# Optimization experiments

Measured on AMD Instinct MI355X. Metric: run time of the kernel, lower is better.

## Reference

```python
import jax, jax.numpy as jnp
import numpy as np

B, S, D, H = 8, 1024, 768, 12
DH = D // H  # 64
PATCHES = S  # module's `patches` arg; rows >= patches//2 are zeroed pre-softmax


def setup_inputs() -> dict:
    key = jax.random.key(0)
    ks = jax.random.split(key, 5)
    sc = 1.0 / np.sqrt(D)
    return {
        "hidden_states": jax.random.normal(ks[0], (B, S, D), dtype=jnp.float32),
        "Wq": jax.random.normal(ks[1], (D, D), dtype=jnp.float32) * sc,
        "bq": jnp.zeros((D,), dtype=jnp.float32),
        "Wk": jax.random.normal(ks[2], (D, D), dtype=jnp.float32) * sc,
        "bk": jnp.zeros((D,), dtype=jnp.float32),
        "Wv": jax.random.normal(ks[3], (D, D), dtype=jnp.float32) * sc,
        "bv": jnp.zeros((D,), dtype=jnp.float32),
        "Wo": jax.random.normal(ks[4], (D, D), dtype=jnp.float32) * sc,
        "bo": jnp.zeros((D,), dtype=jnp.float32),
    }


def _split_heads(x):
    # [B,S,D] -> [B,H,S,DH]
    b, s, _ = x.shape
    return x.reshape(b, s, H, DH).transpose(0, 2, 1, 3)


def reference(hidden_states, Wq, bq, Wk, bk, Wv, bv, Wo, bo):
    # self-attention path (kv=None), mask=None path, eval-mode dropout (identity)
    q = _split_heads(hidden_states @ Wq + bq)
    k = _split_heads(hidden_states @ Wk + bk)
    v = _split_heads(hidden_states @ Wv + bv)
    scores = jnp.einsum("bhqd,bhkd->bhqk", q, k) / np.sqrt(DH)
    # custom masking: zero out all score rows for query positions >= patches//2
    scores = scores.at[:, :, PATCHES // 2 :, :].set(0.0)
    probs = jax.nn.softmax(scores, axis=-1)
    ctx = jnp.einsum("bhqk,bhkd->bhqd", probs, v)
    ctx = ctx.transpose(0, 2, 1, 3).reshape(hidden_states.shape[0], -1, D)
    return ctx @ Wo + bo  # vis=False -> weights not returned
```

## Files before the change

### kernel.cpp

```cpp
#include <hip/hip_runtime.h>
#include <hip/hip_bf16.h>
#include <cstdint>


typedef __bf16 bf16_t;
typedef bf16_t bf16x8 __attribute__((ext_vector_type(8)));
typedef float f32x4 __attribute__((ext_vector_type(4)));

#define QSCALE 0.18033688011112042f

__device__ __forceinline__ f32x4 mfma16(bf16x8 a, bf16x8 b, f32x4 c) {
  return __builtin_amdgcn_mfma_f32_16x16x32_bf16(a, b, c, 0, 0, 0);
}
__device__ __forceinline__ unsigned packbf(float x, float y) {
  union { bf16_t h; unsigned short u; } a, b;
  a.h = (bf16_t)x; b.h = (bf16_t)y;
  return (unsigned)a.u | ((unsigned)b.u << 16);
}
__device__ __forceinline__ unsigned short tobf(float x) {
  union { bf16_t h; unsigned short u; } a; a.h = (bf16_t)x; return a.u;
}
__device__ __forceinline__ void glds16(const void* g, void* s) {
  __builtin_amdgcn_global_load_lds((const __attribute__((address_space(1))) void*)g,
                                   (__attribute__((address_space(3))) void*)s, 16, 0, 0);
}

__global__ __launch_bounds__(256) void k_prep(const float* __restrict__ X,
                                              const float* __restrict__ Wq,
                                              const float* __restrict__ Wk,
                                              const float* __restrict__ Wv,
                                              const float* __restrict__ Wo,
                                              unsigned short* __restrict__ Xbf,
                                              unsigned short* __restrict__ Wt) {
  __shared__ float tile[64][65];
  if (blockIdx.x < 3072) {
    int i = blockIdx.x * 256 + threadIdx.x;
    const float4* p = (const float4*)X;
    float4 a = p[2 * i], b = p[2 * i + 1];
    uint4 o;
    o.x = packbf(a.x, a.y); o.y = packbf(a.z, a.w);
    o.z = packbf(b.x, b.y); o.w = packbf(b.z, b.w);
    ((uint4*)Xbf)[i] = o;
    return;
  }
  int id = blockIdx.x - 3072;
  int which = id / 144;
  int rem = id - which * 144;
  const float* W = (which == 0) ? Wq : (which == 1) ? Wk : (which == 2) ? Wv : Wo;
  int k0 = (rem / 12) * 64, n0 = (rem % 12) * 64;
  int t = threadIdx.x;
  int c = t & 63, r0 = t >> 6;
#pragma unroll
  for (int i = 0; i < 16; ++i) {
    int r = r0 + i * 4;
    tile[r][c] = W[(size_t)(k0 + r) * 768 + n0 + c];
  }
  __syncthreads();
#pragma unroll
  for (int i = 0; i < 16; ++i) {
    int nr = r0 + i * 4;
    Wt[(size_t)(which * 768 + n0 + nr) * 768 + k0 + c] = tobf(tile[c][nr]);
  }
}

__global__ __launch_bounds__(256) void k_gemm_qkv(
    const unsigned short* __restrict__ Xbf, const unsigned short* __restrict__ Wt,
    const float* __restrict__ bq, const float* __restrict__ bk, const float* __restrict__ bv,
    unsigned short* __restrict__ Qw, unsigned short* __restrict__ Kw,
    unsigned short* __restrict__ Vt) {
  __shared__ __align__(16) unsigned short As0[4096], Bs0[4096], As1[4096], Bs1[4096];
  int id = blockIdx.x;
  int mt, nt;
  if (id < 576) { int mf = id / 18; mt = ((mf >> 2) << 3) + (mf & 3); nt = id - mf * 18; }
  else { int j = id - 576; int mh = j / 12; mt = ((mh >> 2) << 3) + 4 + (mh & 3); nt = 6 + (j - mh * 12); }
  const int m0 = mt * 128, n0 = nt * 128;
  const int tid = threadIdx.x, w = tid >> 6, l = tid & 63, lr = l & 15, lg = l >> 4;
  const int wm = w >> 1, wn = w & 1;
  const unsigned short* gA = Xbf + (size_t)(m0 + (tid >> 2)) * 768 + (tid & 3) * 8;
  const unsigned short* gB = Wt + (size_t)(n0 + (tid >> 2)) * 768 + (tid & 3) * 8;
  const int woff = w * 512;
  const int rAo = (wm * 64 + lr) * 32 + lg * 8;
  const int rBo = (wn * 64 + lr) * 32 + lg * 8;
  f32x4 acc[4][4] = {};

#define QKV_STAGE(bufA, bufB, ko)                                              \
  {                                                                            \
    glds16(gA + (ko), bufA + woff);                                            \
    glds16(gA + 64 * 768 + (ko), bufA + woff + 2048);                          \
    glds16(gB + (ko), bufB + woff);                                            \
    glds16(gB + 64 * 768 + (ko), bufB + woff + 2048);                          \
  }
#define QKV_COMPUTE(bufA, bufB)                                                \
  {                                                                            \
    bf16x8 af[4], bfr[4];                                                      \
    _Pragma("unroll") for (int i = 0; i < 4; ++i)                              \
      af[i] = *(const bf16x8*)(bufA + rAo + i * 512);                          \
    _Pragma("unroll") for (int i = 0; i < 4; ++i)                              \
      bfr[i] = *(const bf16x8*)(bufB + rBo + i * 512);                         \
    _Pragma("unroll") for (int i = 0; i < 4; ++i)                              \
      _Pragma("unroll") for (int j = 0; j < 4; ++j)                            \
        acc[i][j] = mfma16(af[i], bfr[j], acc[i][j]);                          \
  }

  QKV_STAGE(As0, Bs0, 0);
  __syncthreads();
  for (int kk = 0; kk < 12; ++kk) {
    const int ko = kk * 64;
    QKV_STAGE(As1, Bs1, ko + 32);
    QKV_COMPUTE(As0, Bs0);
    __syncthreads();
    if (kk < 11) { QKV_STAGE(As0, Bs0, ko + 64); }
    QKV_COMPUTE(As1, Bs1);
    __syncthreads();
  }
#undef QKV_STAGE
#undef QKV_COMPUTE

  const int rbase = m0 + wm * 64 + lg * 4;
  const int cbase = n0 + wn * 64 + lr;
#pragma unroll
  for (int nf = 0; nf < 4; ++nf) {
    const int n = cbase + nf * 16;
#pragma unroll
    for (int mf = 0; mf < 4; ++mf) {
      const int r = rbase + mf * 16;
      const int b = r >> 10, s = r & 1023;
      if (n < 768) {
        const int h = n >> 6, dh = n & 63;
        const float bias = bq[n];
        unsigned short* qp = Qw + ((size_t)(b * 12 + h) * 512 + s) * 64 + dh;
#pragma unroll
        for (int rg = 0; rg < 4; ++rg)
          qp[(size_t)rg * 64] = tobf((acc[mf][nf][rg] + bias) * QSCALE);
      } else if (n < 1536) {
        const int d = n - 768, h = d >> 6, dh = d & 63;
        const float bias = bk[d];
        unsigned short* kp = Kw + ((size_t)(b * 12 + h) * 1024 + s) * 64 + dh;
#pragma unroll
        for (int rg = 0; rg < 4; ++rg)
          kp[(size_t)rg * 64] = tobf(acc[mf][nf][rg] + bias);
      } else {
        const int d = n - 1536, h = d >> 6, dh = d & 63;
        const float bias = bv[d];
        uint2 pv;
        pv.x = packbf(acc[mf][nf][0] + bias, acc[mf][nf][1] + bias);
        pv.y = packbf(acc[mf][nf][2] + bias, acc[mf][nf][3] + bias);
        *(uint2*)(Vt + ((size_t)(b * 12 + h) * 64 + dh) * 1024 + s) = pv;
      }
    }
  }
}

__global__ __launch_bounds__(256) void k_attn(const unsigned short* __restrict__ Qw,
                                              const unsigned short* __restrict__ Kw,
                                              const unsigned short* __restrict__ Vt,
                                              unsigned short* __restrict__ Ctx,
                                              float* __restrict__ mv) {
  const int id = blockIdx.x;
  const int bh = id % 96;
  const int q0 = (id / 96) * 64;
  const int tid = threadIdx.x, w = tid >> 6, l = tid & 63, lr = l & 15, lg = l >> 4;
  const unsigned short* Qp = Qw + (size_t)bh * 512 * 64;
  const unsigned short* Kp = Kw + (size_t)bh * 1024 * 64;
  const unsigned short* Vp = Vt + (size_t)bh * 64 * 1024;

  __shared__ __align__(16) unsigned short Ks[2][4096];
  __shared__ __align__(16) unsigned short Vs[2][4096];
  __shared__ __align__(16) unsigned short P[4 * 16 * 72];

  const int j1 = 2 * w, j2 = 2 * w + 1;
  const int rA = j1 * 8 + (l >> 3), cA = (l & 7) ^ (rA & 7);
  const int rB = j2 * 8 + (l >> 3), cB = (l & 7) ^ (rB & 7);
  const unsigned short* kSrcA = Kp + rA * 64 + cA * 8;
  const unsigned short* kSrcB = Kp + rB * 64 + cB * 8;
  const unsigned short* vSrcA = Vp + rA * 1024 + cA * 8;
  const unsigned short* vSrcB = Vp + rB * 1024 + cB * 8;

  const int s0 = lr * 64 + ((lg ^ (lr & 7)) * 8);
  const int s1 = lr * 64 + (((lg + 4) ^ (lr & 7)) * 8);

  unsigned short* prow = P + (w * 16 + lr) * 72;
  const unsigned short* prd = prow + lg * 8;
  const int qrow = q0 + w * 16 + lr;
  const bf16x8 qf0 = *(const bf16x8*)(Qp + (size_t)qrow * 64 + lg * 8);
  const bf16x8 qf1 = *(const bf16x8*)(Qp + (size_t)qrow * 64 + 32 + lg * 8);

  f32x4 accc[4] = {};
  float vs0 = 0.f, vs1 = 0.f, vs2 = 0.f, vs3 = 0.f;
  float z = 0.f;

  glds16(kSrcA, &Ks[0][j1 * 512]);
  glds16(kSrcB, &Ks[0][j2 * 512]);
  glds16(vSrcA, &Vs[0][j1 * 512]);
  glds16(vSrcB, &Vs[0][j2 * 512]);
  __syncthreads();

  for (int t = 0; t < 16; ++t) {
    const int pcur = t & 1;
    if (t < 15) {
      const int kv0 = (t + 1) * 64;
      glds16(kSrcA + (size_t)kv0 * 64, &Ks[1 - pcur][j1 * 512]);
      glds16(kSrcB + (size_t)kv0 * 64, &Ks[1 - pcur][j2 * 512]);
      glds16(vSrcA + kv0, &Vs[1 - pcur][j1 * 512]);
      glds16(vSrcB + kv0, &Vs[1 - pcur][j2 * 512]);
    }
    const unsigned short* Kb = Ks[pcur];
    const unsigned short* Vb = Vs[pcur];
    f32x4 ss[4] = {};
#pragma unroll
    for (int m = 0; m < 4; ++m) {
      bf16x8 k0 = *(const bf16x8*)(Kb + m * 1024 + s0);
      bf16x8 k1 = *(const bf16x8*)(Kb + m * 1024 + s1);
      ss[m] = mfma16(k0, qf0, ss[m]);
      ss[m] = mfma16(k1, qf1, ss[m]);
    }
#pragma unroll
    for (int m = 0; m < 4; ++m) {
      float p0 = exp2f(ss[m][0]), p1 = exp2f(ss[m][1]);
      float p2 = exp2f(ss[m][2]), p3 = exp2f(ss[m][3]);
      z += (p0 + p1) + (p2 + p3);
      uint2 pw;
      pw.x = packbf(p0, p1); pw.y = packbf(p2, p3);
      *(uint2*)(prow + m * 16 + lg * 4) = pw;
    }
    bf16x8 pb0 = *(const bf16x8*)prd;
    bf16x8 pb1 = *(const bf16x8*)(prd + 32);
#pragma unroll
    for (int m = 0; m < 4; ++m) {
      bf16x8 v0 = *(const bf16x8*)(Vb + m * 1024 + s0);
      bf16x8 v1 = *(const bf16x8*)(Vb + m * 1024 + s1);
      if (id < 96) {
        float sv = 0.f;
#pragma unroll
        for (int jj = 0; jj < 8; ++jj) sv += (float)v0[jj] + (float)v1[jj];
        if (m == 0) vs0 += sv; else if (m == 1) vs1 += sv;
        else if (m == 2) vs2 += sv; else vs3 += sv;
      }
      accc[m] = mfma16(v0, pb0, accc[m]);
      accc[m] = mfma16(v1, pb1, accc[m]);
    }
    __syncthreads();
  }

  const int b = bh / 12, h = bh - b * 12;
  if (id < 96) {
    vs0 += __shfl_xor(vs0, 16, 64); vs0 += __shfl_xor(vs0, 32, 64);
    vs1 += __shfl_xor(vs1, 16, 64); vs1 += __shfl_xor(vs1, 32, 64);
    vs2 += __shfl_xor(vs2, 16, 64); vs2 += __shfl_xor(vs2, 32, 64);
    vs3 += __shfl_xor(vs3, 16, 64); vs3 += __shfl_xor(vs3, 32, 64);
    if (w == 0 && lg == 0) {
      float* mp = mv + b * 768 + h * 64 + lr;
      mp[0] = vs0 * (1.f / 1024.f);
      mp[16] = vs1 * (1.f / 1024.f);
      mp[32] = vs2 * (1.f / 1024.f);
      mp[48] = vs3 * (1.f / 1024.f);
    }
  }

  z += __shfl_xor(z, 16, 64);
  z += __shfl_xor(z, 32, 64);
  const float zinv = 1.0f / z;
  unsigned short* crow = Ctx + ((size_t)b * 512 + qrow) * 768 + h * 64 + lg * 4;
#pragma unroll
  for (int m = 0; m < 4; ++m) {
    uint2 pv;
    pv.x = packbf(accc[m][0] * zinv, accc[m][1] * zinv);
    pv.y = packbf(accc[m][2] * zinv, accc[m][3] * zinv);
    *(uint2*)(crow + m * 16) = pv;
  }
}

__global__ __launch_bounds__(256) void k_gemm_o(const unsigned short* __restrict__ Ctx,
                                                const unsigned short* __restrict__ WtO,
                                                const float* __restrict__ mv,
                                                const float* __restrict__ Wo,
                                                const float* __restrict__ bo,
                                                float* __restrict__ out) {
  __shared__ __align__(16) unsigned short As0[4096], Bs0[4096], As1[4096], Bs1[4096];
  __shared__ float mvs[768];
  __shared__ float cvals[128];
  const int tid = threadIdx.x;
  if (blockIdx.x >= 192) {
    const int tb = blockIdx.x - 192;
    const int b = tb / 6, n0 = (tb - b * 6) * 128;
    for (int i = tid; i < 768; i += 256) mvs[i] = mv[b * 768 + i];
    __syncthreads();
    const int col = n0 + (tid >> 1);
    const int half = tid & 1;
    float a = 0.f;
    const int kend = half * 384 + 384;
    for (int k = half * 384; k < kend; ++k)
      a += mvs[k] * Wo[(size_t)k * 768 + col];
    a += __shfl_xor(a, 1, 64);
    if (half == 0) cvals[col - n0] = a + bo[col];
    __syncthreads();
    const float4 c4 = ((const float4*)cvals)[tid & 31];
    const int srow = tid >> 5;
    float* obase = out + ((size_t)b * 1024 + 512 + srow) * 768 + n0;
    for (int r = 0; r < 512; r += 8)
      ((float4*)(obase + (size_t)r * 768))[tid & 31] = c4;
    return;
  }
  const int m0 = (blockIdx.x / 6) * 128, n0 = (blockIdx.x % 6) * 128;
  const int w = tid >> 6, l = tid & 63, lr = l & 15, lg = l >> 4;
  const int wm = w >> 1, wn = w & 1;
  const unsigned short* gA = Ctx + (size_t)(m0 + (tid >> 2)) * 768 + (tid & 3) * 8;
  const unsigned short* gB = WtO + (size_t)(n0 + (tid >> 2)) * 768 + (tid & 3) * 8;
  const int woff = w * 512;
  const int rAo = (wm * 64 + lr) * 32 + lg * 8;
  const int rBo = (wn * 64 + lr) * 32 + lg * 8;
  f32x4 acc[4][4] = {};

#define O_STAGE(bufA, bufB, ko)                                                \
  {                                                                            \
    glds16(gA + (ko), bufA + woff);                                            \
    glds16(gA + 64 * 768 + (ko), bufA + woff + 2048);                          \
    glds16(gB + (ko), bufB + woff);                                            \
    glds16(gB + 64 * 768 + (ko), bufB + woff + 2048);                          \
  }
#define O_COMPUTE(bufA, bufB)                                                  \
  {                                                                            \
    bf16x8 af[4], bfr[4];                                                      \
    _Pragma("unroll") for (int i = 0; i < 4; ++i)                              \
      af[i] = *(const bf16x8*)(bufA + rAo + i * 512);                          \
    _Pragma("unroll") for (int i = 0; i < 4; ++i)                              \
      bfr[i] = *(const bf16x8*)(bufB + rBo + i * 512);                         \
    _Pragma("unroll") for (int i = 0; i < 4; ++i)                              \
      _Pragma("unroll") for (int j = 0; j < 4; ++j)                            \
        acc[i][j] = mfma16(af[i], bfr[j], acc[i][j]);                          \
  }

  O_STAGE(As0, Bs0, 0);
  __syncthreads();
  for (int kk = 0; kk < 12; ++kk) {
    const int ko = kk * 64;
    O_STAGE(As1, Bs1, ko + 32);
    O_COMPUTE(As0, Bs0);
    __syncthreads();
    if (kk < 11) { O_STAGE(As0, Bs0, ko + 64); }
    O_COMPUTE(As1, Bs1);
    __syncthreads();
  }
#undef O_STAGE
#undef O_COMPUTE

  const int rbase = m0 + wm * 64 + lg * 4;
  const int cbase = n0 + wn * 64 + lr;
#pragma unroll
  for (int nf = 0; nf < 4; ++nf) {
    const int n = cbase + nf * 16;
    const float bias = bo[n];
#pragma unroll
    for (int mf = 0; mf < 4; ++mf) {
      const int r = rbase + mf * 16;
      const int b = r >> 9, s = r & 511;
      float* op = out + ((size_t)b * 1024 + s) * 768 + n;
#pragma unroll
      for (int rg = 0; rg < 4; ++rg) op[(size_t)rg * 768] = acc[mf][nf][rg] + bias;
    }
  }
}

extern "C" void kernel_launch(void* const* d_in, const int* in_sizes, int n_in,
                              void* d_out, int out_size, void* d_ws, size_t ws_size,
                              hipStream_t stream) {
  const float* X  = (const float*)d_in[0];
  const float* Wq = (const float*)d_in[1];
  const float* bq = (const float*)d_in[2];
  const float* Wk = (const float*)d_in[3];
  const float* bk = (const float*)d_in[4];
  const float* Wv = (const float*)d_in[5];
  const float* bv = (const float*)d_in[6];
  const float* Wo = (const float*)d_in[7];
  const float* bo = (const float*)d_in[8];
  float* out = (float*)d_out;
  char* ws = (char*)d_ws;

  unsigned short* Xbf = (unsigned short*)(ws);
  unsigned short* Wt  = (unsigned short*)(ws + 12582912);
  unsigned short* Qw  = (unsigned short*)(ws + 17301504);
  unsigned short* Kw  = (unsigned short*)(ws + 23592960);
  unsigned short* Vt  = (unsigned short*)(ws + 36175872);
  unsigned short* Ctx = (unsigned short*)(ws + 48758784);
  float* mv   = (float*)(ws + 55050240);

  k_prep<<<3648, 256, 0, stream>>>(X, Wq, Wk, Wv, Wo, Xbf, Wt);
  k_gemm_qkv<<<960, 256, 0, stream>>>(Xbf, Wt, bq, bk, bv, Qw, Kw, Vt);
  k_attn<<<768, 256, 0, stream>>>(Qw, Kw, Vt, Ctx, mv);
  k_gemm_o<<<240, 256, 0, stream>>>(Ctx, Wt + (size_t)2304 * 768, mv, Wo, bo, out);
}
```

Measured before the change: 201.6 us.

## Replace double-buffered QKV GEMM loop with single-buffer K=64 stages; add MFMA priority hints

The QKV projection GEMM drops its ping-pong double buffering. It now loads a full 64-wide K slab (two 32-wide halves) into one shared buffer per iteration, with barriers before and after compute. This halves the iteration count and the staging bookkeeping, but global-to-LDS loads no longer overlap MFMA work within a block and must rely on other resident blocks for latency hiding. Separately, the attention loop raises wave priority with s_setprio around its MFMA sections, so matrix work is issued ahead of competing waves.

```diff
diff --git a/kernel.cpp b/kernel.cpp
--- a/kernel.cpp
+++ b/kernel.cpp
@@ -68,7 +68,7 @@
     const float* __restrict__ bq, const float* __restrict__ bk, const float* __restrict__ bv,
     unsigned short* __restrict__ Qw, unsigned short* __restrict__ Kw,
     unsigned short* __restrict__ Vt) {
-  __shared__ __align__(16) unsigned short As0[4096], Bs0[4096], As1[4096], Bs1[4096];
+  __shared__ __align__(16) unsigned short As[8192], Bs[8192];
   int id = blockIdx.x;
   int mt, nt;
   if (id < 576) { int mf = id / 18; mt = ((mf >> 2) << 3) + (mf & 3); nt = id - mf * 18; }
@@ -76,46 +76,35 @@
   const int m0 = mt * 128, n0 = nt * 128;
   const int tid = threadIdx.x, w = tid >> 6, l = tid & 63, lr = l & 15, lg = l >> 4;
   const int wm = w >> 1, wn = w & 1;
-  const unsigned short* gA = Xbf + (size_t)(m0 + (tid >> 2)) * 768 + (tid & 3) * 8;
-  const unsigned short* gB = Wt + (size_t)(n0 + (tid >> 2)) * 768 + (tid & 3) * 8;
-  const int woff = w * 512;
-  const int rAo = (wm * 64 + lr) * 32 + lg * 8;
-  const int rBo = (wn * 64 + lr) * 32 + lg * 8;
+  const unsigned short* gA = Xbf + (size_t)(m0 + (l >> 2)) * 768 + (l & 3) * 8;
+  const unsigned short* gB = Wt + (size_t)(n0 + (l >> 2)) * 768 + (l & 3) * 8;
+  const size_t rlo = (size_t)(w * 16) * 768, rhi = (size_t)((4 + w) * 16) * 768;
+  unsigned short* sA0 = As + w * 512;
+  unsigned short* sB0 = Bs + w * 512;
+  const unsigned short* rA = As + (wm * 64 + lr) * 32 + lg * 8;
+  const unsigned short* rB = Bs + (wn * 64 + lr) * 32 + lg * 8;
   f32x4 acc[4][4] = {};
-
-#define QKV_STAGE(bufA, bufB, ko)                                              \
-  {                                                                            \
-    glds16(gA + (ko), bufA + woff);                                            \
-    glds16(gA + 64 * 768 + (ko), bufA + woff + 2048);                          \
-    glds16(gB + (ko), bufB + woff);                                            \
-    glds16(gB + 64 * 768 + (ko), bufB + woff + 2048);                          \
-  }
-#define QKV_COMPUTE(bufA, bufB)                                                \
-  {                                                                            \
-    bf16x8 af[4], bfr[4];                                                      \
-    _Pragma("unroll") for (int i = 0; i < 4; ++i)                              \
-      af[i] = *(const bf16x8*)(bufA + rAo + i * 512);                          \
-    _Pragma("unroll") for (int i = 0; i < 4; ++i)                              \
-      bfr[i] = *(const bf16x8*)(bufB + rBo + i * 512);                         \
-    _Pragma("unroll") for (int i = 0; i < 4; ++i)                              \
-      _Pragma("unroll") for (int j = 0; j < 4; ++j)                            \
-        acc[i][j] = mfma16(af[i], bfr[j], acc[i][j]);                          \
-  }
-
-  QKV_STAGE(As0, Bs0, 0);
-  __syncthreads();
-  for (int kk = 0; kk < 12; ++kk) {
-    const int ko = kk * 64;
-    QKV_STAGE(As1, Bs1, ko + 32);
-    QKV_COMPUTE(As0, Bs0);
-    __syncthreads();
-    if (kk < 11) { QKV_STAGE(As0, Bs0, ko + 64); }
-    QKV_COMPUTE(As1, Bs1);
-    __syncthreads();
-  }
-#undef QKV_STAGE
-#undef QKV_COMPUTE
-
+  for (int kt = 0; kt < 12; ++kt) {
+    const int ko = kt * 64;
+    glds16(gA + rlo + ko, sA0);            glds16(gA + rhi + ko, sA0 + 2048);
+    glds16(gA + rlo + ko + 32, sA0 + 4096); glds16(gA + rhi + ko + 32, sA0 + 6144);
+    glds16(gB + rlo + ko, sB0);            glds16(gB + rhi + ko, sB0 + 2048);
+    glds16(gB + rlo + ko + 32, sB0 + 4096); glds16(gB + rhi + ko + 32, sB0 + 6144);
+    __syncthreads();
+#pragma unroll
+    for (int kh = 0; kh < 2; ++kh) {
+      bf16x8 af[4], bfr[4];
+#pragma unroll
+      for (int i = 0; i < 4; ++i) af[i] = *(const bf16x8*)(rA + kh * 4096 + i * 512);
+#pragma unroll
+      for (int i = 0; i < 4; ++i) bfr[i] = *(const bf16x8*)(rB + kh * 4096 + i * 512);
+#pragma unroll
+      for (int i = 0; i < 4; ++i)
+#pragma unroll
+        for (int j = 0; j < 4; ++j) acc[i][j] = mfma16(af[i], bfr[j], acc[i][j]);
+    }
+    __syncthreads();
+  }
   const int rbase = m0 + wm * 64 + lg * 4;
   const int cbase = n0 + wn * 64 + lr;
 #pragma unroll
@@ -207,6 +196,7 @@
     const unsigned short* Kb = Ks[pcur];
     const unsigned short* Vb = Vs[pcur];
     f32x4 ss[4] = {};
+    __builtin_amdgcn_s_setprio(1);
 #pragma unroll
     for (int m = 0; m < 4; ++m) {
       bf16x8 k0 = *(const bf16x8*)(Kb + m * 1024 + s0);
@@ -214,6 +204,7 @@
       ss[m] = mfma16(k0, qf0, ss[m]);
       ss[m] = mfma16(k1, qf1, ss[m]);
     }
+    __builtin_amdgcn_s_setprio(0);
 #pragma unroll
     for (int m = 0; m < 4; ++m) {
       float p0 = exp2f(ss[m][0]), p1 = exp2f(ss[m][1]);
@@ -225,6 +216,7 @@
     }
     bf16x8 pb0 = *(const bf16x8*)prd;
     bf16x8 pb1 = *(const bf16x8*)(prd + 32);
+    __builtin_amdgcn_s_setprio(1);
 #pragma unroll
     for (int m = 0; m < 4; ++m) {
       bf16x8 v0 = *(const bf16x8*)(Vb + m * 1024 + s0);
@@ -239,6 +231,7 @@
       accc[m] = mfma16(v0, pb0, accc[m]);
       accc[m] = mfma16(v1, pb1, accc[m]);
     }
+    __builtin_amdgcn_s_setprio(0);
     __syncthreads();
   }
 
```

Result: no change. 199.7 us (-1.0%).
